# Optimization experiments

Measured on AMD Instinct MI355X. Metric: run time of the kernel, lower is better.

## Reference

```python
import jax, jax.numpy as jnp
import numpy as np

FOCAL = 1015.0
H = 500
W = 500
NV = 5023
NF = 9976
B = 2
AMB, DIF, SPEC, SHIN = 0.5, 0.3, 0.2, 64.0  # pytorch3d PointLights/Materials defaults
EPS = 1e-6


def _vertex_normals(verts, faces):
    # verts [V,3] float, faces [F,3] int -> [V,3] unit normals (area-weighted scatter-add)
    v0 = verts[faces[:, 0]]
    v1 = verts[faces[:, 1]]
    v2 = verts[faces[:, 2]]
    n = jnp.zeros_like(verts)
    n = n.at[faces[:, 1]].add(jnp.cross(v2 - v1, v0 - v1))
    n = n.at[faces[:, 2]].add(jnp.cross(v0 - v2, v1 - v2))
    n = n.at[faces[:, 0]].add(jnp.cross(v1 - v0, v2 - v0))
    return n / jnp.maximum(jnp.linalg.norm(n, axis=-1, keepdims=True), EPS)


def _render_one(verts_w, faces, normals_w):
    # world->camera: look_at_view_transform(1,0,0) gives R=diag(-1,1,-1); T overridden to 0
    verts_c = verts_w * jnp.array([-1.0, 1.0, -1.0], dtype=verts_w.dtype)
    x, y, z = verts_c[:, 0], verts_c[:, 1], verts_c[:, 2]
    zs = jnp.maximum(z, EPS)
    # screen-space (non-NDC) pinhole projection, principal point at image center,
    # pytorch3d camera convention: +X left, +Y up -> pixel coords decrease
    px = W / 2.0 - FOCAL * x / zs
    py = H / 2.0 - FOCAL * y / zs
    i0, i1, i2 = faces[:, 0], faces[:, 1], faces[:, 2]
    ax, ay, za = px[i0], py[i0], z[i0]
    bx, by, zb = px[i1], py[i1], z[i1]
    cx, cy, zc = px[i2], py[i2], z[i2]
    denom = (by - cy) * (ax - cx) + (cx - bx) * (ay - cy)
    valid = (jnp.abs(denom) >= EPS) & (za > EPS) & (zb > EPS) & (zc > EPS)
    denom = jnp.where(valid, denom, 1.0)
    xs = jnp.arange(W, dtype=jnp.float32) + 0.5

    def row(carry, yi):
        # hard z-buffer rasterization of one pixel row against all faces
        yp = yi.astype(jnp.float32) + 0.5
        dx = xs[:, None] - cx[None, :]  # [W,F]
        dy = yp - cy                    # [F]
        w0 = ((by - cy)[None] * dx + (cx - bx)[None] * dy[None]) / denom[None]
        w1 = ((cy - ay)[None] * dx + (ax - cx)[None] * dy[None]) / denom[None]
        w2 = 1.0 - w0 - w1
        inside = (w0 >= 0) & (w1 >= 0) & (w2 >= 0) & valid[None]
        zpix = jnp.where(inside, w0 * za + w1 * zb + w2 * zc, jnp.inf)
        f = jnp.argmin(zpix, axis=1)  # faces_per_pixel=1, blur_radius=0 -> hard nearest face
        mask = jnp.isfinite(jnp.min(zpix, axis=1))
        take = lambda w: jnp.take_along_axis(w, f[:, None], axis=1)[:, 0]
        return carry, (f, take(w0), take(w1), take(w2), mask)

    _, (fidx, b0, b1, b2, mask) = jax.lax.scan(jax.checkpoint(row), 0, jnp.arange(H))
    bary = jnp.stack([b0, b1, b2], -1)      # [H,W,3] screen-space barycentrics
    tri = faces[fidx]                        # [H,W,3] vertex ids of hit face
    p = jnp.einsum('hwk,hwkc->hwc', bary, verts_w[tri])    # interpolated world position
    n = jnp.einsum('hwk,hwkc->hwc', bary, normals_w[tri])  # interpolated normal
    n = n / jnp.maximum(jnp.linalg.norm(n, axis=-1, keepdims=True), EPS)
    # SoftPhongShader: point light at world origin; camera center also at origin (T=0)
    l = -p / jnp.maximum(jnp.linalg.norm(p, axis=-1, keepdims=True), EPS)
    ndl = jnp.maximum(jnp.sum(n * l, -1, keepdims=True), 0.0)
    refl = 2.0 * jnp.sum(l * n, -1, keepdims=True) * n - l
    vdr = jnp.maximum(jnp.sum(l * refl, -1, keepdims=True), 0.0)
    shade = 0.5 * (AMB + DIF * ndl) + SPEC * vdr ** SHIN  # verts_rgb = 0.5 everywhere
    rgb = jnp.where(mask[..., None], jnp.broadcast_to(shade, (H, W, 3)), 1.0)  # white bg
    rgba = jnp.concatenate([rgb, mask[..., None].astype(rgb.dtype)], -1)
    return jnp.clip(rgba, 0.0, 255.0)


def setup_inputs():
    key = jax.random.key(0)
    k1, k2 = jax.random.split(key)
    verts = jax.random.normal(k1, (B, NV, 3), dtype=jnp.float32) * 0.05
    verts = verts.at[..., 2].add(-0.6)  # mesh in front of camera (z_cam = -z_world)
    faces = jax.random.randint(k2, (NF, 3), 0, NV, dtype=jnp.int32)
    return {"rott_geometry": verts, "faces": faces}


def reference(rott_geometry, faces):
    normals = jax.vmap(_vertex_normals, in_axes=(0, None))(rott_geometry, faces)
    return jax.vmap(_render_one, in_axes=(0, None, 0))(rott_geometry, faces, normals)
```

## Files before the change

### kernel.cpp

```cpp
#include <hip/hip_runtime.h>
#include <math.h>

namespace {

constexpr int kH = 500, kW = 500, kNV = 5023, kNF = 9976, kB = 2;
constexpr float kFocal = 1015.0f;
constexpr float kEps = 1e-6f;
constexpr int kNB = 8;
constexpr int kChunks = 8;
constexpr int kFPC = kNF / kChunks;
constexpr unsigned kListCap = 1800000u;

__device__ inline void cross3(float ax, float ay, float az,
                              float bx, float by, float bz,
                              float& cx, float& cy, float& cz) {
  cx = ay * bz - az * by;
  cy = az * bx - ax * bz;
  cz = ax * by - ay * bx;
}

__device__ inline bool tileCull(const float4 r0, const float4 r1,
                                float tX0, float tX1, float tY0, float tY1) {
  float hi0 = fmaf(r0.x, r0.x >= 0.f ? tX1 : tX0,
                   fmaf(r0.y, r0.y >= 0.f ? tY1 : tY0, r0.z));
  float lo0 = fmaf(r0.x, r0.x >= 0.f ? tX0 : tX1,
                   fmaf(r0.y, r0.y >= 0.f ? tY0 : tY1, r0.z));
  float hi1 = fmaf(r1.x, r1.x >= 0.f ? tX1 : tX0,
                   fmaf(r1.y, r1.y >= 0.f ? tY1 : tY0, r1.z));
  float lo1 = fmaf(r1.x, r1.x >= 0.f ? tX0 : tX1,
                   fmaf(r1.y, r1.y >= 0.f ? tY0 : tY1, r1.z));
  float m2 = 2.f * r0.w;
  return hi0 >= -m2 && hi1 >= -m2 && (1.f - lo0 - lo1) >= -m2;
}

__device__ inline int bucketOf(float zminf, float zlo, float iscale) {
  float t = (zminf - zlo) * iscale;
  t = fminf(fmaxf(t, 0.f), (float)(kNB - 1));
  return (int)t;
}

__device__ inline void projectV(const float* __restrict__ vb, int vi,
                                float& px, float& py, float& zc) {
  float vx = vb[3 * vi], vy = vb[3 * vi + 1], vz = vb[3 * vi + 2];
  float xc = -vx, yc = vy;
  zc = -vz;
  float zs = fmaxf(zc, kEps);
  px = __fsub_rn(0.5f * kW, __fdiv_rn(__fmul_rn(kFocal, xc), zs));
  py = __fsub_rn(0.5f * kH, __fdiv_rn(__fmul_rn(kFocal, yc), zs));
}

__global__ void setup_k(const float* __restrict__ verts,
                        const int* __restrict__ faces,
                        float* __restrict__ nacc,
                        float4* __restrict__ fdE,
                        float4* __restrict__ fdP,
                        unsigned* __restrict__ tb,
                        unsigned* __restrict__ zr) {
  int f = blockIdx.x * 256 + threadIdx.x;
  int b = blockIdx.y;
  bool act = (f < kNF);
  float redMin = INFINITY, redMax = 0.0f;
  if (act) {
    size_t idx = (size_t)b * kNF + f;
    const float* vb = verts + (size_t)b * kNV * 3;
    int i0 = faces[3 * f + 0], i1 = faces[3 * f + 1], i2 = faces[3 * f + 2];
    {
      float x0 = vb[3 * i0], y0 = vb[3 * i0 + 1], z0 = vb[3 * i0 + 2];
      float x1 = vb[3 * i1], y1 = vb[3 * i1 + 1], z1 = vb[3 * i1 + 2];
      float x2 = vb[3 * i2], y2 = vb[3 * i2 + 1], z2 = vb[3 * i2 + 2];
      float* nb = nacc + (size_t)b * kNV * 3;
      float cx, cy, cz;
      cross3(x2 - x1, y2 - y1, z2 - z1, x0 - x1, y0 - y1, z0 - z1, cx, cy, cz);
      atomicAdd(nb + 3 * i1 + 0, cx);
      atomicAdd(nb + 3 * i1 + 1, cy);
      atomicAdd(nb + 3 * i1 + 2, cz);
      cross3(x0 - x2, y0 - y2, z0 - z2, x1 - x2, y1 - y2, z1 - z2, cx, cy, cz);
      atomicAdd(nb + 3 * i2 + 0, cx);
      atomicAdd(nb + 3 * i2 + 1, cy);
      atomicAdd(nb + 3 * i2 + 2, cz);
      cross3(x1 - x0, y1 - y0, z1 - z0, x2 - x0, y2 - y0, z2 - z0, cx, cy, cz);
      atomicAdd(nb + 3 * i0 + 0, cx);
      atomicAdd(nb + 3 * i0 + 1, cy);
      atomicAdd(nb + 3 * i0 + 2, cz);
    }
    float ax, ay, za, bx, by, zb, cx, cy, zc;
    projectV(vb, i0, ax, ay, za);
    projectV(vb, i1, bx, by, zb);
    projectV(vb, i2, cx, cy, zc);
    float A0 = __fsub_rn(by, cy);
    float B0 = __fsub_rn(cx, bx);
    float A1 = __fsub_rn(cy, ay);
    float B1 = __fsub_rn(ax, cx);
    float e = __fsub_rn(ay, cy);
    float den = __fadd_rn(__fmul_rn(A0, B1), __fmul_rn(B0, e));
    bool valid =
        (fabsf(den) >= kEps) && (za > kEps) && (zb > kEps) && (zc > kEps);
    float ds = valid ? den : 1.0f;

    float4* oe = fdE + idx * 3;
    oe[0] = make_float4(cx, cy, A0, B0);
    oe[1] = make_float4(A1, B1, ds, za);
    oe[2] = make_float4(zb, zc, 0.0f, 0.0f);

    float P0 = A0 / ds, Q0 = B0 / ds, R0 = -(A0 * cx + B0 * cy) / ds;
    float P1 = A1 / ds, Q1 = B1 / ds, R1 = -(A1 * cx + B1 * cy) / ds;
    float dza = za - zc, dzb = zb - zc;
    float Zx = dza * P0 + dzb * P1;
    float Zy = dza * Q0 + dzb * Q1;
    float Zc = dza * R0 + dzb * R1 + zc;
    float S0 = (fabsf(P0) + fabsf(Q0)) * 512.f + fabsf(R0);
    float S1 = (fabsf(P1) + fabsf(Q1)) * 512.f + fabsf(R1);
    float Sz = (fabsf(Zx) + fabsf(Zy)) * 512.f + fabsf(Zc);
    float m0 = S0 * 0x1p-18f;
    float m1 = S1 * 0x1p-18f;
    float mw = m0 + m1 + 2e-6f;
    float mz = m0 * fabsf(dza) + m1 * fabsf(dzb) + Sz * 0x1p-18f +
               0x1p-18f * (fabsf(zc) + fabsf(dza) + fabsf(dzb) + 1.f) + 2e-6f;
    float zminf = fminf(fminf(za, zb), zc);

    float4* op = fdP + idx * 3;
    op[0] = make_float4(P0, Q0, R0, mw);
    op[1] = make_float4(P1, Q1, R1, mz);
    op[2] = make_float4(Zx, Zy, Zc, zminf);

    unsigned pack;
    if (valid) {
      float mnx = fminf(fminf(ax, bx), cx) - 0.5f;
      float mxx = fmaxf(fmaxf(ax, bx), cx) + 0.5f;
      float mny = fminf(fminf(ay, by), cy) - 0.5f;
      float mxy = fmaxf(fmaxf(ay, by), cy) + 0.5f;
      float c0 = fminf(fmaxf(ceilf((mnx - 15.5f) * 0.0625f), 0.f), 31.f);
      float c1 = fminf(fmaxf(floorf((mxx - 0.5f) * 0.0625f), 0.f), 31.f);
      float r0 = fminf(fmaxf(ceilf((mny - 15.5f) * 0.0625f), 0.f), 31.f);
      float r1 = fminf(fmaxf(floorf((mxy - 0.5f) * 0.0625f), 0.f), 31.f);
      unsigned uc0 = (unsigned)c0, uc1 = (unsigned)c1;
      unsigned ur0 = (unsigned)r0, ur1 = (unsigned)r1;
      if (mxx < mnx || mxy < mny) { uc0 = 1; uc1 = 0; }
      pack = uc0 | (uc1 << 8) | (ur0 << 16) | (ur1 << 24);
      redMin = zminf;
      redMax = zminf;
    } else {
      pack = 1u;
    }
    tb[idx] = pack;
  }
#pragma unroll
  for (int d = 32; d >= 1; d >>= 1) {
    redMin = fminf(redMin, __shfl_xor(redMin, d, 64));
    redMax = fmaxf(redMax, __shfl_xor(redMax, d, 64));
  }
  if ((threadIdx.x & 63) == 0 && redMin < INFINITY) {
    atomicMin(zr + b, __float_as_uint(redMin));
    atomicMax(zr + 2 + b, __float_as_uint(redMax));
  }
}

__global__ __launch_bounds__(256) void bin_k(
    const float4* __restrict__ fdP, const unsigned* __restrict__ tb,
    unsigned* __restrict__ zr, unsigned* __restrict__ cnt,
    unsigned short* __restrict__ list) {
  __shared__ unsigned lc[256];
  __shared__ unsigned segBase;
  int c = blockIdx.x, ty = blockIdx.y, b = blockIdx.z;
  size_t bOff = (size_t)b * kNF;
  int t = threadIdx.x;
  lc[t] = 0u;
  __syncthreads();

  float tY0 = 16.f * ty + 0.5f, tY1 = tY0 + 15.f;
  float zlo = __uint_as_float(zr[b]);
  float zhi = __uint_as_float(zr[2 + b]);
  float range = zhi - zlo;
  float iscale = range > 1e-30f ? (float)kNB / range : 0.f;
  int f0 = c * kFPC, f1 = min(kNF, f0 + kFPC);

  for (int f = f0 + t; f < f1; f += 256) {
    unsigned pk = tb[bOff + f];
    int cx0 = pk & 0xFF, cx1 = (pk >> 8) & 0xFF;
    int ry0 = (pk >> 16) & 0xFF, ry1 = (pk >> 24) & 0xFF;
    if (ty < ry0 || ty > ry1 || cx0 > cx1) continue;
    const float4* rp = fdP + (bOff + f) * 3;
    float4 r0 = rp[0], r1 = rp[1], r2 = rp[2];
    int q = bucketOf(r2.w, zlo, iscale);
    for (int tx = cx0; tx <= cx1; ++tx) {
      float tX0 = 16.f * tx + 0.5f, tX1 = tX0 + 15.f;
      if (tileCull(r0, r1, tX0, tX1, tY0, tY1))
        atomicAdd(&lc[tx * kNB + q], 1u);
    }
  }
  __syncthreads();

  unsigned own = lc[t];
  for (int d = 1; d < 256; d <<= 1) {
    unsigned w = (t >= d) ? lc[t - d] : 0u;
    __syncthreads();
    lc[t] += w;
    __syncthreads();
  }
  unsigned excl = lc[t] - own;
  unsigned tot = lc[255];
  if (t == 0) segBase = atomicAdd(&zr[4], tot);
  __syncthreads();
  unsigned sb = segBase;

  unsigned blk = ((unsigned)(b * 32 + ty) * kChunks + (unsigned)c);
  cnt[blk * 257 + t] = sb + excl;
  if (t == 0) cnt[blk * 257 + 256] = sb + tot;
  __syncthreads();
  lc[t] = sb + excl;
  __syncthreads();

  for (int f = f0 + t; f < f1; f += 256) {
    unsigned pk = tb[bOff + f];
    int cx0 = pk & 0xFF, cx1 = (pk >> 8) & 0xFF;
    int ry0 = (pk >> 16) & 0xFF, ry1 = (pk >> 24) & 0xFF;
    if (ty < ry0 || ty > ry1 || cx0 > cx1) continue;
    const float4* rp = fdP + (bOff + f) * 3;
    float4 r0 = rp[0], r1 = rp[1], r2 = rp[2];
    int q = bucketOf(r2.w, zlo, iscale);
    for (int tx = cx0; tx <= cx1; ++tx) {
      float tX0 = 16.f * tx + 0.5f, tX1 = tX0 + 15.f;
      if (tileCull(r0, r1, tX0, tX1, tY0, tY1)) {
        unsigned pos = atomicAdd(&lc[tx * kNB + q], 1u);
        if (pos < kListCap) list[pos] = (unsigned short)f;
      }
    }
  }
}

__global__ __launch_bounds__(256) void raster_k(
    const float4* __restrict__ fdP, const float4* __restrict__ fdE,
    const unsigned* __restrict__ cnt, const unsigned short* __restrict__ list,
    const unsigned* __restrict__ zr, const float* __restrict__ verts,
    const float* __restrict__ nacc, const int* __restrict__ faces,
    float* __restrict__ out) {
  __shared__ float4 sA[256], sB[256], sC[256];
  __shared__ unsigned sOff[kChunks * 9];
  int b = blockIdx.z;
  size_t bOff = (size_t)b * kNF;
  int t = threadIdx.x;
  int tx = t & 15, ty = t >> 4;
  int x = blockIdx.x * 16 + tx;
  int y = blockIdx.y * 16 + ty;
  float xp = (float)x + 0.5f;
  float yp = (float)y + 0.5f;
  bool live = (x < kW && y < kH);
  float zmin = live ? INFINITY : -INFINITY;
  int best = 0x7FFFFFFF;
  float bw0 = 0.f, bw1 = 0.f, bw2 = 0.f;

  float zlo = __uint_as_float(zr[b]);
  float zhi = __uint_as_float(zr[2 + b]);
  float range = zhi - zlo;
  float bwid = range > 1e-30f ? range * (1.f / kNB) : 0.f;

  if (t < kChunks * 9) {
    int c = t / 9, j = t - c * 9;
    unsigned blk = ((unsigned)(b * 32 + blockIdx.y) * kChunks + (unsigned)c);
    sOff[t] = cnt[blk * 257 + blockIdx.x * 8 + j];
  }
  __syncthreads();

  for (int q = 0; q < kNB; ++q) {
    if (q > 0) {
      float lb = zlo + (float)q * bwid * (1.f - 1e-5f) - 2e-5f;
      if (__syncthreads_and(zmin < lb)) break;
    }
    unsigned st[kChunks], pre[kChunks + 1];
    pre[0] = 0;
#pragma unroll
    for (int c = 0; c < kChunks; ++c) {
      unsigned s0 = sOff[c * 9 + q], e0 = sOff[c * 9 + q + 1];
      st[c] = s0;
      pre[c + 1] = pre[c] + (e0 - s0);
    }
    unsigned m = pre[kChunks];
    for (unsigned base = 0; base < m; base += 256) {
      int n = min(256u, m - base);
      __syncthreads();
      if (t < n) {
        unsigned idx = base + t, src = 0;
#pragma unroll
        for (int c = 0; c < kChunks; ++c)
          if (idx >= pre[c] && idx < pre[c + 1]) src = st[c] + (idx - pre[c]);
        unsigned fi = list[src];
        const float4* rp = fdP + (bOff + fi) * 3;
        float4 r0 = rp[0], r1 = rp[1], r2 = rp[2];
        r2.w = __int_as_float((int)fi);
        sA[t] = r0;
        sB[t] = r1;
        sC[t] = r2;
      }
      __syncthreads();
      for (int k = 0; k < n; ++k) {
        float4 a = sA[k], bq = sB[k], c = sC[k];
        float w0a = fmaf(a.x, xp, fmaf(a.y, yp, a.z));
        float w1a = fmaf(bq.x, xp, fmaf(bq.y, yp, bq.z));
        float w2a = 1.f - w0a - w1a;
        float zl = fmaf(c.x, xp, fmaf(c.y, yp, c.z));
        float wmin = fminf(fminf(w0a, w1a), w2a);
        if (wmin >= -a.w && zl <= zmin + bq.w) {
          int fi = __float_as_int(c.w);
          const float4* ep = fdE + (bOff + fi) * 3;
          float4 e0 = ep[0], e1 = ep[1], e2 = ep[2];
          float dx = __fsub_rn(xp, e0.x), dy = __fsub_rn(yp, e0.y);
          float num0 = __fadd_rn(__fmul_rn(e0.z, dx), __fmul_rn(e0.w, dy));
          float num1 = __fadd_rn(__fmul_rn(e1.x, dx), __fmul_rn(e1.y, dy));
          float w0 = __fdiv_rn(num0, e1.z);
          float w1 = __fdiv_rn(num1, e1.z);
          float w2 = __fsub_rn(__fsub_rn(1.f, w0), w1);
          if (w0 >= 0.f && w1 >= 0.f && w2 >= 0.f) {
            float z = __fadd_rn(
                __fadd_rn(__fmul_rn(w0, e1.w), __fmul_rn(w1, e2.x)),
                __fmul_rn(w2, e2.y));
            if (z < zmin || (z == zmin && fi < best)) {
              zmin = z; best = fi; bw0 = w0; bw1 = w1; bw2 = w2;
            }
          }
        }
      }
    }
  }

  if (!live) return;

  float rv, av;
  if (zmin < INFINITY) {
    int i0 = faces[3 * best + 0], i1 = faces[3 * best + 1], i2 = faces[3 * best + 2];
    const float* vb = verts + (size_t)b * kNV * 3;
    const float* nb = nacc + (size_t)b * kNV * 3;
    float n0x = nb[3 * i0], n0y = nb[3 * i0 + 1], n0z = nb[3 * i0 + 2];
    float n1x = nb[3 * i1], n1y = nb[3 * i1 + 1], n1z = nb[3 * i1 + 2];
    float n2x = nb[3 * i2], n2y = nb[3 * i2 + 1], n2z = nb[3 * i2 + 2];
    float d0 = fmaxf(sqrtf(n0x * n0x + n0y * n0y + n0z * n0z), kEps);
    float d1 = fmaxf(sqrtf(n1x * n1x + n1y * n1y + n1z * n1z), kEps);
    float d2 = fmaxf(sqrtf(n2x * n2x + n2y * n2y + n2z * n2z), kEps);
    n0x /= d0; n0y /= d0; n0z /= d0;
    n1x /= d1; n1y /= d1; n1z /= d1;
    n2x /= d2; n2y /= d2; n2z /= d2;
    float px_ = bw0 * vb[3 * i0 + 0] + bw1 * vb[3 * i1 + 0] + bw2 * vb[3 * i2 + 0];
    float py_ = bw0 * vb[3 * i0 + 1] + bw1 * vb[3 * i1 + 1] + bw2 * vb[3 * i2 + 1];
    float pz_ = bw0 * vb[3 * i0 + 2] + bw1 * vb[3 * i1 + 2] + bw2 * vb[3 * i2 + 2];
    float nx = bw0 * n0x + bw1 * n1x + bw2 * n2x;
    float ny = bw0 * n0y + bw1 * n1y + bw2 * n2y;
    float nz = bw0 * n0z + bw1 * n1z + bw2 * n2z;
    float nn = sqrtf(nx * nx + ny * ny + nz * nz);
    float nd = fmaxf(nn, kEps);
    nx /= nd; ny /= nd; nz /= nd;
    float pn = sqrtf(px_ * px_ + py_ * py_ + pz_ * pz_);
    float pd = fmaxf(pn, kEps);
    float lx = -px_ / pd, ly = -py_ / pd, lz = -pz_ / pd;
    float sdot = nx * lx + ny * ly + nz * lz;
    float ndl = fmaxf(sdot, 0.0f);
    float rx = 2.0f * sdot * nx - lx;
    float ry = 2.0f * sdot * ny - ly;
    float rz = 2.0f * sdot * nz - lz;
    float vdr = fmaxf(lx * rx + ly * ry + lz * rz, 0.0f);
    float qv = vdr;
    qv = qv * qv; qv = qv * qv; qv = qv * qv;
    qv = qv * qv; qv = qv * qv; qv = qv * qv;
    float shade = 0.5f * (0.5f + 0.3f * ndl) + 0.2f * qv;
    rv = fminf(fmaxf(shade, 0.0f), 255.0f);
    av = 1.0f;
  } else {
    rv = 1.0f;
    av = 0.0f;
  }
  ((float4*)out)[((size_t)b * kH + y) * kW + x] = make_float4(rv, rv, rv, av);
}

}

extern "C" void kernel_launch(void* const* d_in, const int* in_sizes, int n_in,
                              void* d_out, int out_size, void* d_ws, size_t ws_size,
                              hipStream_t stream) {
  (void)in_sizes; (void)n_in; (void)out_size; (void)ws_size;
  const float* verts = (const float*)d_in[0];
  const int* faces = (const int*)d_in[1];
  float* out = (float*)d_out;
  float* ws = (float*)d_ws;

  float* nacc = ws;
  float4* fdE = (float4*)(ws + 71680);
  float4* fdP = (float4*)(ws + 311296);
  unsigned* tb = (unsigned*)(ws + 550912);
  unsigned* zr = (unsigned*)(ws + 570880);
  unsigned* cnt = (unsigned*)(ws + 571008);
  unsigned short* list = (unsigned short*)(ws + 702720);

  hipMemsetAsync(nacc, 0, (size_t)kB * kNV * 3 * sizeof(float), stream);
  hipMemsetAsync(zr, 0xFF, 2 * sizeof(unsigned), stream);
  hipMemsetAsync(zr + 2, 0x00, 3 * sizeof(unsigned), stream);

  hipLaunchKernelGGL(setup_k, dim3((kNF + 255) / 256, kB), dim3(256), 0,
                     stream, verts, faces, nacc, fdE, fdP, tb, zr);
  hipLaunchKernelGGL(bin_k, dim3(kChunks, 32, kB), dim3(256), 0,
                     stream, fdP, tb, zr, cnt, list);
  hipLaunchKernelGGL(raster_k, dim3(32, 32, kB), dim3(256), 0, stream,
                     fdP, fdE, cnt, list, zr, verts, nacc, faces, out);
}
```

Before: 151.5 us.

## Split raster face lists across two blocks and merge via 64-bit atomicMin

Each screen tile is now rasterized by two blocks, each taking alternating entries of the binned face list, doubling the grid. Per-pixel results are packed into a (depth, face) 64-bit key and merged with atomicMin into the output buffer, which is pre-filled with 0xFF. A new shade kernel then recomputes barycentrics from the winning face and does the shading. This is meant to raise parallelism in the raster stage, at the cost of an extra memset, an extra kernel launch, global atomics, and weaker early-out culling because each block sees only half the faces.

```diff
diff --git a/kernel.cpp b/kernel.cpp
--- a/kernel.cpp
+++ b/kernel.cpp
@@ -9,6 +9,7 @@
 constexpr int kNB = 8;
 constexpr int kChunks = 8;
 constexpr int kFPC = kNF / kChunks;
+constexpr int kSplit = 2;
 constexpr unsigned kListCap = 1800000u;
 
 __device__ inline void cross3(float ax, float ay, float az,
@@ -231,12 +232,11 @@
 __global__ __launch_bounds__(256) void raster_k(
     const float4* __restrict__ fdP, const float4* __restrict__ fdE,
     const unsigned* __restrict__ cnt, const unsigned short* __restrict__ list,
-    const unsigned* __restrict__ zr, const float* __restrict__ verts,
-    const float* __restrict__ nacc, const int* __restrict__ faces,
-    float* __restrict__ out) {
+    const unsigned* __restrict__ zr, unsigned long long* __restrict__ keys) {
   __shared__ float4 sA[256], sB[256], sC[256];
   __shared__ unsigned sOff[kChunks * 9];
-  int b = blockIdx.z;
+  int bz = blockIdx.z;
+  int b = bz >> 1, s = bz & 1;
   size_t bOff = (size_t)b * kNF;
   int t = threadIdx.x;
   int tx = t & 15, ty = t >> 4;
@@ -247,7 +247,6 @@
   bool live = (x < kW && y < kH);
   float zmin = live ? INFINITY : -INFINITY;
   int best = 0x7FFFFFFF;
-  float bw0 = 0.f, bw1 = 0.f, bw2 = 0.f;
 
   float zlo = __uint_as_float(zr[b]);
   float zhi = __uint_as_float(zr[2 + b]);
@@ -275,11 +274,12 @@
       pre[c + 1] = pre[c] + (e0 - s0);
     }
     unsigned m = pre[kChunks];
-    for (unsigned base = 0; base < m; base += 256) {
-      int n = min(256u, m - base);
+    unsigned mS = (m > (unsigned)s) ? (m - s + 1) >> 1 : 0u;
+    for (unsigned base = 0; base < mS; base += 256) {
+      int n = min(256u, mS - base);
       __syncthreads();
       if (t < n) {
-        unsigned idx = base + t, src = 0;
+        unsigned idx = (base + t) * 2 + s, src = 0;
 #pragma unroll
         for (int c = 0; c < kChunks; ++c)
           if (idx >= pre[c] && idx < pre[c + 1]) src = st[c] + (idx - pre[c]);
@@ -313,20 +313,46 @@
             float z = __fadd_rn(
                 __fadd_rn(__fmul_rn(w0, e1.w), __fmul_rn(w1, e2.x)),
                 __fmul_rn(w2, e2.y));
-            if (z < zmin || (z == zmin && fi < best)) {
-              zmin = z; best = fi; bw0 = w0; bw1 = w1; bw2 = w2;
-            }
+            if (z < zmin || (z == zmin && fi < best)) { zmin = z; best = fi; }
           }
         }
       }
     }
   }
 
-  if (!live) return;
-
+  if (live && zmin < INFINITY) {
+    unsigned long long key =
+        ((unsigned long long)__float_as_uint(zmin) << 32) | (unsigned)best;
+    atomicMin(&keys[(((size_t)b * kH + y) * kW + x) * 2], key);
+  }
+}
+
+__global__ void shade_k(const float4* __restrict__ fdE,
+                        const float* __restrict__ verts,
+                        const float* __restrict__ nacc,
+                        const int* __restrict__ faces,
+                        float* __restrict__ out) {
+  int p = blockIdx.x * 256 + threadIdx.x;
+  if (p >= kB * kH * kW) return;
+  int b = p / (kH * kW);
+  int r = p - b * kH * kW;
+  int y = r / kW, x = r - y * kW;
+  unsigned long long key = ((const unsigned long long*)out)[(size_t)p * 2];
   float rv, av;
-  if (zmin < INFINITY) {
-    int i0 = faces[3 * best + 0], i1 = faces[3 * best + 1], i2 = faces[3 * best + 2];
+  if (key == ~0ull) {
+    rv = 1.0f; av = 0.0f;
+  } else {
+    int fi = (int)(key & 0xFFFFFFFFull);
+    float xp = (float)x + 0.5f, yp = (float)y + 0.5f;
+    const float4* ep = fdE + ((size_t)b * kNF + fi) * 3;
+    float4 e0 = ep[0], e1 = ep[1];
+    float dx = __fsub_rn(xp, e0.x), dy = __fsub_rn(yp, e0.y);
+    float num0 = __fadd_rn(__fmul_rn(e0.z, dx), __fmul_rn(e0.w, dy));
+    float num1 = __fadd_rn(__fmul_rn(e1.x, dx), __fmul_rn(e1.y, dy));
+    float w0 = __fdiv_rn(num0, e1.z);
+    float w1 = __fdiv_rn(num1, e1.z);
+    float w2 = __fsub_rn(__fsub_rn(1.f, w0), w1);
+    int i0 = faces[3 * fi + 0], i1 = faces[3 * fi + 1], i2 = faces[3 * fi + 2];
     const float* vb = verts + (size_t)b * kNV * 3;
     const float* nb = nacc + (size_t)b * kNV * 3;
     float n0x = nb[3 * i0], n0y = nb[3 * i0 + 1], n0z = nb[3 * i0 + 2];
@@ -338,12 +364,12 @@
     n0x /= d0; n0y /= d0; n0z /= d0;
     n1x /= d1; n1y /= d1; n1z /= d1;
     n2x /= d2; n2y /= d2; n2z /= d2;
-    float px_ = bw0 * vb[3 * i0 + 0] + bw1 * vb[3 * i1 + 0] + bw2 * vb[3 * i2 + 0];
-    float py_ = bw0 * vb[3 * i0 + 1] + bw1 * vb[3 * i1 + 1] + bw2 * vb[3 * i2 + 1];
-    float pz_ = bw0 * vb[3 * i0 + 2] + bw1 * vb[3 * i1 + 2] + bw2 * vb[3 * i2 + 2];
-    float nx = bw0 * n0x + bw1 * n1x + bw2 * n2x;
-    float ny = bw0 * n0y + bw1 * n1y + bw2 * n2y;
-    float nz = bw0 * n0z + bw1 * n1z + bw2 * n2z;
+    float px_ = w0 * vb[3 * i0 + 0] + w1 * vb[3 * i1 + 0] + w2 * vb[3 * i2 + 0];
+    float py_ = w0 * vb[3 * i0 + 1] + w1 * vb[3 * i1 + 1] + w2 * vb[3 * i2 + 1];
+    float pz_ = w0 * vb[3 * i0 + 2] + w1 * vb[3 * i1 + 2] + w2 * vb[3 * i2 + 2];
+    float nx = w0 * n0x + w1 * n1x + w2 * n2x;
+    float ny = w0 * n0y + w1 * n1y + w2 * n2y;
+    float nz = w0 * n0z + w1 * n1z + w2 * n2z;
     float nn = sqrtf(nx * nx + ny * ny + nz * nz);
     float nd = fmaxf(nn, kEps);
     nx /= nd; ny /= nd; nz /= nd;
@@ -362,11 +388,8 @@
     float shade = 0.5f * (0.5f + 0.3f * ndl) + 0.2f * qv;
     rv = fminf(fmaxf(shade, 0.0f), 255.0f);
     av = 1.0f;
-  } else {
-    rv = 1.0f;
-    av = 0.0f;
-  }
-  ((float4*)out)[((size_t)b * kH + y) * kW + x] = make_float4(rv, rv, rv, av);
+  }
+  ((float4*)out)[p] = make_float4(rv, rv, rv, av);
 }
 
 }
@@ -391,11 +414,14 @@
   hipMemsetAsync(nacc, 0, (size_t)kB * kNV * 3 * sizeof(float), stream);
   hipMemsetAsync(zr, 0xFF, 2 * sizeof(unsigned), stream);
   hipMemsetAsync(zr + 2, 0x00, 3 * sizeof(unsigned), stream);
+  hipMemsetAsync(out, 0xFF, (size_t)kB * kH * kW * 16, stream);
 
   hipLaunchKernelGGL(setup_k, dim3((kNF + 255) / 256, kB), dim3(256), 0,
                      stream, verts, faces, nacc, fdE, fdP, tb, zr);
   hipLaunchKernelGGL(bin_k, dim3(kChunks, 32, kB), dim3(256), 0,
                      stream, fdP, tb, zr, cnt, list);
-  hipLaunchKernelGGL(raster_k, dim3(32, 32, kB), dim3(256), 0, stream,
-                     fdP, fdE, cnt, list, zr, verts, nacc, faces, out);
-}
+  hipLaunchKernelGGL(raster_k, dim3(32, 32, kB * kSplit), dim3(256), 0, stream,
+                     fdP, fdE, cnt, list, zr, (unsigned long long*)out);
+  hipLaunchKernelGGL(shade_k, dim3((kB * kH * kW + 255) / 256), dim3(256), 0,
+                     stream, fdE, verts, nacc, faces, out);
+}
```

After: 193.1 us. 27.4% more time.
